# Kernel optimization log

Hardware: AMD Instinct MI355X
Metric: run time of the kernel (lower is better)

Reference implementation:

```python
import jax, jax.numpy as jnp
import numpy as np

JACCARD_THRESH = 0.5
NEG_POS = 3
VAR0, VAR1 = 0.1, 0.2
MAX_POS = 256  # static cap on gathered positives for the metric-learning terms


def point_form(boxes):
    # (cx,cy,w,h) -> (xmin,ymin,xmax,ymax)
    return jnp.concatenate([boxes[:, :2] - boxes[:, 2:] / 2,
                            boxes[:, :2] + boxes[:, 2:] / 2], axis=1)


def jaccard(a, b):
    # a: [O,4], b: [D,4] point form
    lt = jnp.maximum(a[:, None, :2], b[None, :, :2])
    rb = jnp.minimum(a[:, None, 2:], b[None, :, 2:])
    wh = jnp.clip(rb - lt, 0.0)
    inter = wh[..., 0] * wh[..., 1]
    area_a = (a[:, 2] - a[:, 0]) * (a[:, 3] - a[:, 1])
    area_b = (b[:, 2] - b[:, 0]) * (b[:, 3] - b[:, 1])
    return inter / (area_a[:, None] + area_b[None, :] - inter)


def encode(matched, priors):
    g_cxcy = ((matched[:, :2] + matched[:, 2:]) / 2 - priors[:, :2]) / (VAR0 * priors[:, 2:])
    g_wh = jnp.log((matched[:, 2:] - matched[:, :2]) / priors[:, 2:]) / VAR1
    return jnp.concatenate([g_cxcy, g_wh], axis=1)


def match_one(truths, labels, poses, priors):
    # standard SSD match (per image)
    ov = jaccard(truths, point_form(priors))          # [O, D]
    best_prior_idx = jnp.argmax(ov, axis=1)           # [O]
    best_truth_ov = jnp.max(ov, axis=0)               # [D]
    best_truth_idx = jnp.argmax(ov, axis=0)           # [D]
    best_truth_ov = best_truth_ov.at[best_prior_idx].set(2.0)
    best_truth_idx = best_truth_idx.at[best_prior_idx].set(jnp.arange(truths.shape[0]))
    matches = truths[best_truth_idx]                  # [D,4]
    conf = labels[best_truth_idx] + 1                 # background=0
    conf = jnp.where(best_truth_ov < JACCARD_THRESH, 0, conf)
    return encode(matches, priors), conf.astype(jnp.int32), poses[best_truth_idx]


def multibox_loss(loc_data, conf_data, line_data, pose_data, dbox_list, targets):
    B, D, C = conf_data.shape
    truths = targets[:, :, 0:4]
    labels = targets[:, :, 4].astype(jnp.int32)
    poses = targets[:, :, 5:8]
    loc_t, conf_t, pose_t = jax.vmap(match_one, in_axes=(0, 0, 0, None))(
        truths, labels, poses, dbox_list)

    pos = conf_t > 0                                  # [B,D]
    posf = pos.astype(loc_data.dtype)

    # smooth-L1 loc loss over positives (sum reduction)
    d = loc_data - loc_t
    sl1 = jnp.where(jnp.abs(d) < 1.0, 0.5 * d * d, jnp.abs(d) - 0.5)
    loss_l = jnp.sum(sl1 * posf[..., None])

    # pose squared-error over positives
    loss_p = jnp.sum((pose_data - pose_t) ** 2 * posf[..., None])

    # per-anchor cross entropy + hard-negative mining (double-argsort rank trick)
    logp = jax.nn.log_softmax(conf_data, axis=-1)
    ce = -jnp.take_along_axis(logp, conf_t[..., None], axis=-1)[..., 0]  # [B,D]
    ce_mined = jnp.where(pos, 0.0, ce)
    loss_idx = jnp.argsort(-ce_mined, axis=1)
    idx_rank = jnp.argsort(loss_idx, axis=1)
    num_pos = jnp.sum(pos.astype(jnp.int32), axis=1, keepdims=True)
    num_neg = jnp.minimum(num_pos * NEG_POS, D)
    neg = idx_rank < num_neg
    loss_c = jnp.sum(ce * (pos | neg).astype(ce.dtype))

    N = jnp.maximum(jnp.sum(posf), 1.0)
    loss_l = loss_l / N
    loss_c = loss_c / N
    loss_p = loss_p / N

    # ---- metric-learning block on gathered positives (static cap) ----
    pos_flat = pos.reshape(-1)
    order = jnp.argsort(jnp.where(pos_flat, 0, 1))[:MAX_POS]  # stable: row-major positives first
    valid = pos_flat[order]                                   # [K]
    emb = line_data.reshape(-1, line_data.shape[-1])[order]   # [K,32] raw embeddings
    lab = conf_t.reshape(-1)[order]                           # [K]
    qp = pose_t.reshape(-1, 3)[order]                         # [K,3]

    # PairMarginMiner / TripletMarginLoss use L2-normalized LpDistance by default
    nemb = emb / jnp.maximum(jnp.linalg.norm(emb, axis=1, keepdims=True), 1e-12)
    sq = jnp.sum((nemb[:, None, :] - nemb[None, :, :]) ** 2, axis=-1)
    dist = jnp.sqrt(jnp.maximum(sq, 1e-12))                   # [K,K]

    K = emb.shape[0]
    eye = jnp.eye(K, dtype=bool)
    vpair = valid[:, None] & valid[None, :] & ~eye
    same = lab[:, None] == lab[None, :]
    pos_pair = vpair & same & (dist > 0.2)   # mined hard positive pairs
    neg_pair = vpair & ~same & (dist < 0.8)  # mined hard negative pairs
    n_pp = jnp.sum(pos_pair)
    n_np = jnp.sum(neg_pair)

    # pairs -> triplets sharing the anchor; TripletMarginLoss(margin=0.2), AvgNonZero reducer
    trip_mask = pos_pair[:, :, None] & neg_pair[:, None, :]           # [K,K,K]
    trip_loss = jax.nn.relu(dist[:, :, None] - dist[:, None, :] + 0.2)
    nz = trip_mask & (trip_loss > 0)
    loss_t = jnp.sum(jnp.where(nz, trip_loss, 0.0)) / jnp.maximum(jnp.sum(nz), 1)

    # Ldesk over mined positive pairs: raw-embedding sq-dist vs pose sq-dist consistency
    e_sq = jnp.sum((emb[:, None, :] - emb[None, :, :]) ** 2, axis=-1)
    q_sq = jnp.sum((qp[:, None, :] - qp[None, :, :]) ** 2, axis=-1)
    desk_sum = jnp.sum(jnp.where(pos_pair, (e_sq - q_sq) ** 2, 0.0))
    npp = jnp.maximum(n_pp, 1).astype(loc_data.dtype)
    Ldesk = desk_sum / npp + loss_t / jnp.maximum(n_pp + n_np, 1)
    Ldesk = Ldesk / npp / 32.0

    return loss_l, loss_c, loss_p, Ldesk, loss_t


def setup_inputs():
    key = jax.random.key(0)
    ks = jax.random.split(key, 10)
    B, D, C, L, O = 32, 8732, 21, 32, 8
    loc_data = jax.random.normal(ks[0], (B, D, 4)) * 0.1
    conf_data = jax.random.normal(ks[1], (B, D, C))
    line_data = jax.random.normal(ks[2], (B, D, L))
    pose_data = jax.random.normal(ks[3], (B, D, 3))
    # default boxes (cx,cy,w,h) in (0,1)
    cxcy = jax.random.uniform(ks[4], (D, 2), minval=0.05, maxval=0.95)
    wh = jax.random.uniform(ks[5], (D, 2), minval=0.05, maxval=0.4)
    dbox_list = jnp.concatenate([cxcy, wh], axis=1)
    # targets: [xmin,ymin,xmax,ymax,label,pose(3),unused]
    mins = jax.random.uniform(ks[6], (B, O, 2), minval=0.0, maxval=0.6)
    sizes = jax.random.uniform(ks[7], (B, O, 2), minval=0.1, maxval=0.4)
    boxes = jnp.concatenate([mins, mins + sizes], axis=-1)
    labs = jax.random.randint(ks[8], (B, O, 1), 0, C - 1).astype(jnp.float32)
    pz = jax.random.normal(ks[9], (B, O, 3))
    targets = jnp.concatenate([boxes, labs, pz, jnp.zeros((B, O, 1))], axis=-1)
    return dict(loc_data=loc_data, conf_data=conf_data, line_data=line_data,
                pose_data=pose_data, dbox_list=dbox_list, targets=targets)


def reference(loc_data, conf_data, line_data, pose_data, dbox_list, targets):
    return multibox_loss(loc_data, conf_data, line_data, pose_data, dbox_list, targets)
```

## Files before the change

### kernel.cpp

```cpp
#include <hip/hip_runtime.h>
#include <cstdint>

#define B 32
#define D 8732
#define C 21
#define L 32
#define O 8
#define NSEGB 16
#define SEGLEN 546
#define NSEG 512
#define MT 576
#define NT 1024
#define PAIRB 128
#define TOPB 32
#define FINTGT (PAIRB + TOPB)

struct Ws {
  const float *loc, *conf, *line, *pose, *dbox, *targets;
  float* out;
  unsigned long long* bpPart;
  double* acc;
  int* ictr;
  int* cnt;
  int* posSlice;
  float* sce;
};

__device__ inline double waveSumD(double v) {
  #pragma unroll
  for (int s = 32; s > 0; s >>= 1) v += __shfl_down(v, s, 64);
  return v;
}

__device__ inline float iou_one(float tx1, float ty1, float tx2, float ty2, float ta,
                                float px1, float py1, float px2, float py2, float areaB) {
  float lx = fmaxf(tx1, px1), ly = fmaxf(ty1, py1);
  float rx = fminf(tx2, px2), ry = fminf(ry = ty2, py2);
  float iw = fmaxf(rx - lx, 0.f), ih = fmaxf(ry - ly, 0.f);
  float inter = iw * ih;
  return inter / (ta + areaB - inter);
}

__global__ __launch_bounds__(256) void k_bp(Ws p) {
  __shared__ float tb[O][4], ta[O];
  __shared__ unsigned long long wm[4][O];
  int g = blockIdx.x, tid = threadIdx.x;
  int lane = tid & 63, wav = tid >> 6;
  int b = g >> 4, s = g & 15;
  int dBeg = s * SEGLEN;
  int dEnd = dBeg + SEGLEN; if (dEnd > D) dEnd = D;
  if (g == 0) {
    if (tid < 9) p.acc[tid] = 0.0;
    if (tid == 9) { p.ictr[0] = 0; p.ictr[1] = 0; }
  }
  if (tid < O) {
    const float* tr = p.targets + ((size_t)b * O + tid) * 9;
    tb[tid][0] = tr[0]; tb[tid][1] = tr[1]; tb[tid][2] = tr[2]; tb[tid][3] = tr[3];
    ta[tid] = (tr[2] - tr[0]) * (tr[3] - tr[1]);
  }
  __syncthreads();
  float bi_[O]; int bd_[O];
  #pragma unroll
  for (int t = 0; t < O; t++) { bi_[t] = 0.f; bd_[t] = 0; }
  for (int d = dBeg + tid; d < dEnd; d += 256) {
    float4 db = *(const float4*)(p.dbox + (size_t)d * 4);
    float px1 = db.x - 0.5f*db.z, py1 = db.y - 0.5f*db.w;
    float px2 = db.x + 0.5f*db.z, py2 = db.y + 0.5f*db.w;
    float areaB = db.z * db.w;
    #pragma unroll
    for (int t = 0; t < O; t++) {
      float lx = fmaxf(tb[t][0], px1), ly = fmaxf(tb[t][1], py1);
      float rx = fminf(tb[t][2], px2), ry = fminf(tb[t][3], py2);
      float iw = fmaxf(rx - lx, 0.f), ih = fmaxf(ry - ly, 0.f);
      float inter = iw * ih;
      float iou = inter / (ta[t] + areaB - inter);
      if (iou > bi_[t]) { bi_[t] = iou; bd_[t] = d; }
    }
  }
  #pragma unroll
  for (int t = 0; t < O; t++) {
    unsigned long long k = ((unsigned long long)__float_as_uint(bi_[t]) << 32)
                         | (unsigned long long)(0xFFFFFFFFu - (unsigned)bd_[t]);
    #pragma unroll
    for (int sft = 32; sft > 0; sft >>= 1) {
      unsigned long long o = __shfl_down(k, sft, 64);
      if (o > k) k = o;
    }
    if (lane == 0) wm[wav][t] = k;
  }
  __syncthreads();
  if (tid < O) {
    unsigned long long k = wm[0][tid];
    #pragma unroll
    for (int w = 1; w < 4; w++) if (wm[w][tid] > k) k = wm[w][tid];
    p.bpPart[(size_t)g * O + tid] = k;
  }
}

struct ShM {
  float tb[O][4], ta[O], tl[O], tp_[O][3];
  unsigned long long bpred[128];
  int bpd[O];
  int plist[256];
  int wcnt[9], wbase[9];
  double wred[9][3];
  int run;
};

__global__ __launch_bounds__(MT, 4) void k_match(Ws p) {
  __shared__ ShM sh;
  int g = blockIdx.x, tid = threadIdx.x;
  int lane = tid & 63, wav = tid >> 6;
  int b = g >> 4, s = g & 15;
  int dBeg = s * SEGLEN;
  int dEnd = dBeg + SEGLEN; if (dEnd > D) dEnd = D;
  int d = dBeg + tid;
  bool act = d < dEnd;

  float x[C];
  if (act) {
    const float* cb = p.conf + ((size_t)b * D + d) * C;
    #pragma unroll
    for (int c = 0; c < C; c++) x[c] = cb[c];
  }
  if (tid < O) {
    const float* tr = p.targets + ((size_t)b * O + tid) * 9;
    sh.tb[tid][0] = tr[0]; sh.tb[tid][1] = tr[1];
    sh.tb[tid][2] = tr[2]; sh.tb[tid][3] = tr[3];
    sh.ta[tid] = (tr[2] - tr[0]) * (tr[3] - tr[1]);
    sh.tl[tid] = tr[4];
    sh.tp_[tid][0] = tr[5]; sh.tp_[tid][1] = tr[6]; sh.tp_[tid][2] = tr[7];
  }
  if (tid < 128)
    sh.bpred[tid] = p.bpPart[((size_t)b * NSEGB + (tid >> 3)) * O + (tid & 7)];
  __syncthreads();
  if (tid < O) {
    unsigned long long k = 0ull;
    #pragma unroll
    for (int s2 = 0; s2 < NSEGB; s2++) {
      unsigned long long kk = sh.bpred[s2 * 8 + tid];
      if (kk > k) k = kk;
    }
    sh.bpd[tid] = (int)(0xFFFFFFFFu - (unsigned)(k & 0xFFFFFFFFull));
  }
  __syncthreads();

  double ll = 0, lp = 0, cp = 0;
  int cls = 0, bi = 0;
  if (act) {
    float4 db = *(const float4*)(p.dbox + (size_t)d * 4);
    float px1 = db.x - 0.5f*db.z, py1 = db.y - 0.5f*db.w;
    float px2 = db.x + 0.5f*db.z, py2 = db.y + 0.5f*db.w;
    float areaB = db.z * db.w;
    float bv = -1.0f;
    #pragma unroll
    for (int t = 0; t < O; t++) {
      float iou = iou_one(sh.tb[t][0], sh.tb[t][1], sh.tb[t][2], sh.tb[t][3],
                          sh.ta[t], px1, py1, px2, py2, areaB);
      if (iou > bv) { bv = iou; bi = t; }
    }
    #pragma unroll
    for (int t = O - 1; t >= 0; t--)
      if (sh.bpd[t] == d) { bi = t; bv = 2.0f; break; }
    cls = (bv < 0.5f) ? 0 : ((int)sh.tl[bi] + 1);
    float m = x[0];
    #pragma unroll
    for (int c = 1; c < C; c++) m = fmaxf(m, x[c]);
    float sm = 0.f;
    #pragma unroll
    for (int c = 0; c < C; c++) sm += __expf(x[c] - m);
    float xc = x[0];
    #pragma unroll
    for (int c = 1; c < C; c++) xc = (cls == c) ? x[c] : xc;
    float ce = m + __logf(sm) - xc;
    size_t bd = (size_t)b * D + d;
    if (cls > 0) {
      cp += ce;
      p.sce[bd] = 0.f;
      float g0 = ((sh.tb[bi][0] + sh.tb[bi][2]) * 0.5f - db.x) / (0.1f * db.z);
      float g1 = ((sh.tb[bi][1] + sh.tb[bi][3]) * 0.5f - db.y) / (0.1f * db.w);
      float g2 = logf((sh.tb[bi][2] - sh.tb[bi][0]) / db.z) / 0.2f;
      float g3 = logf((sh.tb[bi][3] - sh.tb[bi][1]) / db.w) / 0.2f;
      float4 lo = *(const float4*)(p.loc + bd * 4);
      float dv, a;
      dv = lo.x - g0; a = fabsf(dv); ll += (double)((a < 1.f) ? 0.5f*dv*dv : a - 0.5f);
      dv = lo.y - g1; a = fabsf(dv); ll += (double)((a < 1.f) ? 0.5f*dv*dv : a - 0.5f);
      dv = lo.z - g2; a = fabsf(dv); ll += (double)((a < 1.f) ? 0.5f*dv*dv : a - 0.5f);
      dv = lo.w - g3; a = fabsf(dv); ll += (double)((a < 1.f) ? 0.5f*dv*dv : a - 0.5f);
      const float* po = p.pose + bd * 3;
      #pragma unroll
      for (int q = 0; q < 3; q++) {
        float pd = po[q] - sh.tp_[bi][q];
        lp += (double)pd * (double)pd;
      }
    } else {
      p.sce[bd] = fmaxf(ce, 0.f);
    }
  }

  const unsigned long long lt = (lane == 0) ? 0ull : (~0ull >> (64 - lane));
  bool pos = act && (cls > 0);
  unsigned long long mm = __ballot(pos);
  if (lane == 0) sh.wcnt[wav] = __popcll(mm);
  __syncthreads();
  if (tid == 0) {
    int r = 0;
    #pragma unroll
    for (int w = 0; w < 9; w++) { sh.wbase[w] = r; r += sh.wcnt[w]; }
    sh.run = r;
  }
  __syncthreads();
  if (pos) {
    int rank = sh.wbase[wav] + __popcll(mm & lt);
    if (rank < 256) sh.plist[rank] = d | (cls << 14) | (bi << 19);
  }
  __syncthreads();
  int tot = sh.run;
  if (tid == 0) p.cnt[g] = tot;
  int stored = (tot < 256) ? tot : 256;
  if (tid < stored) p.posSlice[g * 256 + tid] = sh.plist[tid];
  double a0 = waveSumD(ll), a1 = waveSumD(lp), a2 = waveSumD(cp);
  if (lane == 0) { sh.wred[wav][0] = a0; sh.wred[wav][1] = a1; sh.wred[wav][2] = a2; }
  __syncthreads();
  if (tid == 0) {
    double tll = 0, tlp = 0, tcp = 0;
    #pragma unroll
    for (int w = 0; w < 9; w++) { tll += sh.wred[w][0]; tlp += sh.wred[w][1]; tcp += sh.wred[w][2]; }
    atomicAdd(&p.acc[0], tll);
    atomicAdd(&p.acc[1], tlp);
    atomicAdd(&p.acc[2], tcp);
    atomicAdd(&p.ictr[0], tot);
  }
}

struct __align__(16) ShT {
  float sce[D];
  int whist[16][256];
  int hist[256];
  int scb[NSEGB];
  int nposS;
  unsigned prefixSh; int kkSh;
  double wsum[16], wcnt2[16];
};
struct ShP {
  float embT[L][256];
  float nembT[L][256];
  float qp_s[256][3];
  int   lab_s[256];
  float sd[2][256];
  int   Pi[NSEG + 1];
  int   wscan[8];
  unsigned long long spm[2][4], snm[2][4];
  double w1[2][4];
  int ppc[2][4], npc[2][4];
  double wS[16], wC[16];
};
struct ShD { int last; };
union Sh2 { ShT t; ShP pr; ShD dd; };

__global__ __launch_bounds__(NT) void k_minefin(Ws p) {
  __shared__ Sh2 sh;
  int g = blockIdx.x, tid = threadIdx.x;
  int lane = tid & 63, wav = tid >> 6;

  if (g >= PAIRB) {
    int bb = g - PAIRB;
    if (tid < NSEGB) sh.t.scb[tid] = p.cnt[bb * NSEGB + tid];
    const float* ce = p.sce + (size_t)bb * D;
    for (int i = tid; i < D / 4; i += NT)
      ((float4*)sh.t.sce)[i] = ((const float4*)ce)[i];
    __syncthreads();
    if (tid == 0) {
      int np = 0;
      #pragma unroll
      for (int q = 0; q < NSEGB; q++) np += sh.t.scb[q];
      sh.t.nposS = np;
    }
    __syncthreads();
    int npos = sh.t.nposS;
    int k = npos * 3; if (k > D) k = D;
    unsigned prefix = 0; int kk = k;
    for (int pass = 0; pass < 4; pass++) {
      int shift = 24 - 8 * pass;
      for (int i = tid; i < 16 * 256; i += NT) ((int*)sh.t.whist)[i] = 0;
      __syncthreads();
      unsigned himask = (pass == 0) ? 0u : (0xFFFFFFFFu << (shift + 8));
      for (int d = tid; d < D; d += NT) {
        unsigned keyb = __float_as_uint(sh.t.sce[d]);
        if ((keyb & himask) == (prefix & himask))
          atomicAdd(&sh.t.whist[wav][(keyb >> shift) & 255], 1);
      }
      __syncthreads();
      if (tid < 256) {
        int h = 0;
        #pragma unroll
        for (int w = 0; w < 16; w++) h += sh.t.whist[w][tid];
        sh.t.hist[tid] = h;
      }
      __syncthreads();
      if (tid < 64) {
        int l = tid;
        int h0 = sh.t.hist[l*4], h1 = sh.t.hist[l*4+1], h2 = sh.t.hist[l*4+2], h3 = sh.t.hist[l*4+3];
        int loc4 = h0 + h1 + h2 + h3;
        int suf = loc4;
        #pragma unroll
        for (int st = 1; st < 64; st <<= 1) {
          int o = __shfl_down(suf, st, 64);
          if (l + st < 64) suf += o;
        }
        int snext = suf - loc4;
        int s3 = snext + h3, s2 = s3 + h2, s1 = s2 + h1, s0 = s1 + h0;
        if (s3 >= kk && snext < kk) { sh.t.prefixSh = prefix | ((unsigned)(l*4+3) << shift); sh.t.kkSh = kk - snext; }
        if (s2 >= kk && s3 < kk)    { sh.t.prefixSh = prefix | ((unsigned)(l*4+2) << shift); sh.t.kkSh = kk - s3; }
        if (s1 >= kk && s2 < kk)    { sh.t.prefixSh = prefix | ((unsigned)(l*4+1) << shift); sh.t.kkSh = kk - s2; }
        if (s0 >= kk && s1 < kk)    { sh.t.prefixSh = prefix | ((unsigned)(l*4+0) << shift); sh.t.kkSh = kk - s1; }
      }
      __syncthreads();
      prefix = sh.t.prefixSh; kk = sh.t.kkSh;
      __syncthreads();
    }
    float T = __uint_as_float(prefix);
    double sgt = 0.0; int cgt = 0;
    for (int d = tid; d < D; d += NT) {
      float v = sh.t.sce[d];
      if (__float_as_uint(v) > prefix) { sgt += (double)v; cgt++; }
    }
    double wv = waveSumD(sgt);
    double wc = waveSumD((double)cgt);
    if (lane == 0) { sh.t.wsum[wav] = wv; sh.t.wcnt2[wav] = wc; }
    __syncthreads();
    if (tid == 0) {
      double tsg = 0, tcg = 0;
      #pragma unroll
      for (int w = 0; w < 16; w++) { tsg += sh.t.wsum[w]; tcg += sh.t.wcnt2[w]; }
      atomicAdd(&p.acc[3], tsg + ((double)k - tcg) * (double)T);
    }
  } else {
    int rgrp = tid >> 9;
    int i = 2 * g + rgrp;
    int t5 = tid & 511, j = t5 & 255, qq = t5 >> 8;

    int v = (tid < NSEG) ? p.cnt[tid] : 0;
    #pragma unroll
    for (int st = 1; st < 64; st <<= 1) {
      int o = __shfl_up(v, st, 64);
      if (lane >= st) v += o;
    }
    if (tid < NSEG && lane == 63) sh.pr.wscan[tid >> 6] = v;
    __syncthreads();
    if (tid < NSEG) {
      int add = 0;
      for (int q = 0; q < (tid >> 6); q++) add += sh.pr.wscan[q];
      sh.pr.Pi[tid + 1] = v + add;
    }
    if (tid == 0) sh.pr.Pi[0] = 0;
    __syncthreads();
    int total = sh.pr.Pi[NSEG];
    int Pc = (total < 256) ? total : 256;

    if (tid < 256) {
      int slot = tid;
      bool val = slot < Pc;
      int cls = 0, dpr = 0, seg = 0;
      float q0 = 0.f, q1 = 0.f, q2 = 0.f;
      if (val) {
        int lo = 0;
        #pragma unroll
        for (int st = 256; st > 0; st >>= 1) {
          int m = lo + st;
          if (m <= NSEG - 1 && sh.pr.Pi[m] <= slot) lo = m;
        }
        seg = lo;
        int idx = slot - sh.pr.Pi[seg];
        if (idx < 256) {
          int packed = p.posSlice[seg * 256 + idx];
          dpr = packed & 0x3FFF;
          cls = (packed >> 14) & 31;
          int bi = (packed >> 19) & 7;
          int bb2 = seg >> 4;
          const float* tr = p.targets + ((size_t)bb2 * O + bi) * 9;
          q0 = tr[5]; q1 = tr[6]; q2 = tr[7];
        } else val = false;
      }
      float nrm2 = 0.f;
      if (val) {
        int bb2 = seg >> 4;
        const float4* e4 = (const float4*)(p.line + ((size_t)bb2 * D + dpr) * L);
        #pragma unroll
        for (int c = 0; c < 8; c++) {
          float4 t4 = e4[c];
          sh.pr.embT[c*4+0][slot] = t4.x; sh.pr.embT[c*4+1][slot] = t4.y;
          sh.pr.embT[c*4+2][slot] = t4.z; sh.pr.embT[c*4+3][slot] = t4.w;
          nrm2 += t4.x*t4.x + t4.y*t4.y + t4.z*t4.z + t4.w*t4.w;
        }
      } else {
        #pragma unroll
        for (int c = 0; c < L; c++) sh.pr.embT[c][slot] = 0.f;
      }
      float inv = 1.f / fmaxf(sqrtf(nrm2), 1e-12f);
      #pragma unroll
      for (int c = 0; c < L; c++) sh.pr.nembT[c][slot] = sh.pr.embT[c][slot] * inv;
      sh.pr.lab_s[slot] = val ? cls : 0;
      sh.pr.qp_s[slot][0] = q0; sh.pr.qp_s[slot][1] = q1; sh.pr.qp_s[slot][2] = q2;
    }
    __syncthreads();

    int li = sh.pr.lab_s[i];
    bool vi = (i < Pc);
    bool pp = false, np = false;
    double dsk = 0.0;
    if (qq == 0) {
      bool vj = (j < Pc);
      float sq = 0.f, esq = 0.f;
      #pragma unroll
      for (int c = 0; c < L; c++) {
        float dn = sh.pr.nembT[c][i] - sh.pr.nembT[c][j];
        sq += dn * dn;
        float de = sh.pr.embT[c][i] - sh.pr.embT[c][j];
        esq += de * de;
      }
      float ddv = sqrtf(fmaxf(sq, 1e-12f));
      sh.pr.sd[rgrp][j] = ddv;
      float qsq = 0.f;
      #pragma unroll
      for (int c = 0; c < 3; c++) {
        float dq = sh.pr.qp_s[i][c] - sh.pr.qp_s[j][c];
        qsq += dq * dq;
      }
      bool vp = vi && vj && (i != j);
      bool same = (li == sh.pr.lab_s[j]);
      pp = vp && same && (ddv > 0.2f);
      np = vp && !same && (ddv < 0.8f);
      float diff = esq - qsq;
      dsk = pp ? (double)diff * (double)diff : 0.0;
    }
    unsigned long long pb = __ballot(pp), nb = __ballot(np);
    double dw = waveSumD(dsk);
    if (lane == 0 && qq == 0) {
      int w4 = wav & 3;
      sh.pr.spm[rgrp][w4] = pb; sh.pr.snm[rgrp][w4] = nb; sh.pr.w1[rgrp][w4] = dw;
      sh.pr.ppc[rgrp][w4] = (int)__popcll(pb); sh.pr.npc[rgrp][w4] = (int)__popcll(nb);
    }
    __syncthreads();
    unsigned long long pmw = sh.pr.spm[rgrp][j >> 6];
    bool pj = (pmw >> (j & 63)) & 1ull;
    float sdj = sh.pr.sd[rgrp][j];
    double ts = 0.0, tc = 0.0;
    if (pj) {
      for (int it = 0; it < 128; it++) {
        int kx = qq + 2 * it;
        unsigned long long nmw = sh.pr.snm[rgrp][kx >> 6];
        if ((nmw >> (kx & 63)) & 1ull) {
          float xv = sdj - sh.pr.sd[rgrp][kx] + 0.2f;
          if (xv > 0.f) { ts += (double)xv; tc += 1.0; }
        }
      }
    }
    ts = waveSumD(ts); tc = waveSumD(tc);
    if (lane == 0) { sh.pr.wS[wav] = ts; sh.pr.wC[wav] = tc; }
    __syncthreads();
    if (tid == 0) {
      double S = 0, Cc = 0;
      #pragma unroll
      for (int w = 0; w < 16; w++) { S += sh.pr.wS[w]; Cc += sh.pr.wC[w]; }
      double dsum = 0; int pcnt = 0, ncnt = 0;
      #pragma unroll
      for (int r = 0; r < 2; r++)
        #pragma unroll
        for (int w = 0; w < 4; w++) {
          dsum += sh.pr.w1[r][w]; pcnt += sh.pr.ppc[r][w]; ncnt += sh.pr.npc[r][w];
        }
      atomicAdd(&p.acc[4], dsum);
      atomicAdd(&p.acc[5], (double)pcnt);
      atomicAdd(&p.acc[6], (double)ncnt);
      atomicAdd(&p.acc[7], S);
      atomicAdd(&p.acc[8], Cc);
    }
  }

  if (tid == 0) {
    asm volatile("s_waitcnt vmcnt(0)" ::: "memory");
    int prev = __hip_atomic_fetch_add(&p.ictr[1], 1, __ATOMIC_RELAXED, __HIP_MEMORY_SCOPE_AGENT);
    sh.dd.last = (prev == FINTGT - 1);
  }
  __syncthreads();
  if (!sh.dd.last) return;
  if (tid == 0) {
    double lossL = __hip_atomic_load(&p.acc[0], __ATOMIC_RELAXED, __HIP_MEMORY_SCOPE_AGENT);
    double lossP = __hip_atomic_load(&p.acc[1], __ATOMIC_RELAXED, __HIP_MEMORY_SCOPE_AGENT);
    double ceP   = __hip_atomic_load(&p.acc[2], __ATOMIC_RELAXED, __HIP_MEMORY_SCOPE_AGENT);
    double ceN   = __hip_atomic_load(&p.acc[3], __ATOMIC_RELAXED, __HIP_MEMORY_SCOPE_AGENT);
    double desk  = __hip_atomic_load(&p.acc[4], __ATOMIC_RELAXED, __HIP_MEMORY_SCOPE_AGENT);
    double npp   = __hip_atomic_load(&p.acc[5], __ATOMIC_RELAXED, __HIP_MEMORY_SCOPE_AGENT);
    double nnp   = __hip_atomic_load(&p.acc[6], __ATOMIC_RELAXED, __HIP_MEMORY_SCOPE_AGENT);
    double tripS = __hip_atomic_load(&p.acc[7], __ATOMIC_RELAXED, __HIP_MEMORY_SCOPE_AGENT);
    double tripC = __hip_atomic_load(&p.acc[8], __ATOMIC_RELAXED, __HIP_MEMORY_SCOPE_AGENT);
    int nTotI    = __hip_atomic_load(&p.ictr[0], __ATOMIC_RELAXED, __HIP_MEMORY_SCOPE_AGENT);
    double N = (nTotI > 0) ? (double)nTotI : 1.0;
    p.out[0] = (float)(lossL / N);
    p.out[1] = (float)((ceP + ceN) / N);
    p.out[2] = (float)(lossP / N);
    double cnt = (tripC > 0.0) ? tripC : 1.0;
    double loss_t = tripS / cnt;
    double nppd = (npp > 0.0) ? npp : 1.0;
    double tot = npp + nnp;
    double denom = (tot > 0.0) ? tot : 1.0;
    double Ldesk = desk / nppd + loss_t / denom;
    Ldesk = Ldesk / nppd / 32.0;
    p.out[3] = (float)Ldesk;
    p.out[4] = (float)loss_t;
  }
}

extern "C" void kernel_launch(void* const* d_in, const int* in_sizes, int n_in,
                              void* d_out, int out_size, void* d_ws, size_t ws_size,
                              hipStream_t stream) {
  char* ws = (char*)d_ws;
  size_t off = 0;
  auto alloc = [&](size_t bytes) -> char* {
    char* q = ws + off;
    off += (bytes + 255) & ~(size_t)255;
    return q;
  };
  Ws p;
  p.loc     = (const float*)d_in[0];
  p.conf    = (const float*)d_in[1];
  p.line    = (const float*)d_in[2];
  p.pose    = (const float*)d_in[3];
  p.dbox    = (const float*)d_in[4];
  p.targets = (const float*)d_in[5];
  p.out     = (float*)d_out;
  p.bpPart   = (unsigned long long*)alloc((size_t)NSEG * O * 8);
  p.acc      = (double*)alloc(16 * 8);
  p.ictr     = (int*)alloc(256);
  p.cnt      = (int*)alloc(NSEG * 4);
  p.posSlice = (int*)alloc((size_t)NSEG * 256 * 4);
  p.sce      = (float*)alloc((size_t)B * D * 4);

  k_bp     <<<NSEG,  256, 0, stream>>>(p);
  k_match  <<<NSEG,  MT,  0, stream>>>(p);
  k_minefin<<<FINTGT, NT, 0, stream>>>(p);
}
```

Measured before the change: 149.3 us.

## Stage conf rows through LDS with coalesced loads; compute normalized embeddings on the fly

In k_match, each thread previously read its own 21-float conf row directly from global memory, a strided uncoalesced pattern. The block now copies the whole segment's conf slab into shared memory with coalesced float2 loads and threads read their rows from LDS. This adds about 46KB of shared memory and lowers the launch-bounds occupancy hint from 4 to 2. In the pair kernel, the normalized embedding copy is replaced by a per-slot inverse norm applied inside the distance loop, which halves shared-memory footprint and reads at the cost of a few extra multiplies.

```diff
diff --git a/kernel.cpp b/kernel.cpp
--- a/kernel.cpp
+++ b/kernel.cpp
@@ -35,7 +35,7 @@
 __device__ inline float iou_one(float tx1, float ty1, float tx2, float ty2, float ta,
                                 float px1, float py1, float px2, float py2, float areaB) {
   float lx = fmaxf(tx1, px1), ly = fmaxf(ty1, py1);
-  float rx = fminf(tx2, px2), ry = fminf(ry = ty2, py2);
+  float rx = fminf(tx2, px2), ry = fminf(ty2, py2);
   float iw = fmaxf(rx - lx, 0.f), ih = fmaxf(ry - ly, 0.f);
   float inter = iw * ih;
   return inter / (ta + areaB - inter);
@@ -69,11 +69,8 @@
     float areaB = db.z * db.w;
     #pragma unroll
     for (int t = 0; t < O; t++) {
-      float lx = fmaxf(tb[t][0], px1), ly = fmaxf(tb[t][1], py1);
-      float rx = fminf(tb[t][2], px2), ry = fminf(tb[t][3], py2);
-      float iw = fmaxf(rx - lx, 0.f), ih = fmaxf(ry - ly, 0.f);
-      float inter = iw * ih;
-      float iou = inter / (ta[t] + areaB - inter);
+      float iou = iou_one(tb[t][0], tb[t][1], tb[t][2], tb[t][3], ta[t],
+                          px1, py1, px2, py2, areaB);
       if (iou > bi_[t]) { bi_[t] = iou; bd_[t] = d; }
     }
   }
@@ -98,6 +95,7 @@
 }
 
 struct ShM {
+  float confS[SEGLEN * C];
   float tb[O][4], ta[O], tl[O], tp_[O][3];
   unsigned long long bpred[128];
   int bpd[O];
@@ -107,22 +105,17 @@
   int run;
 };
 
-__global__ __launch_bounds__(MT, 4) void k_match(Ws p) {
+__global__ __launch_bounds__(MT, 2) void k_match(Ws p) {
   __shared__ ShM sh;
   int g = blockIdx.x, tid = threadIdx.x;
   int lane = tid & 63, wav = tid >> 6;
   int b = g >> 4, s = g & 15;
   int dBeg = s * SEGLEN;
   int dEnd = dBeg + SEGLEN; if (dEnd > D) dEnd = D;
+  int segLen = dEnd - dBeg;
   int d = dBeg + tid;
-  bool act = d < dEnd;
-
-  float x[C];
-  if (act) {
-    const float* cb = p.conf + ((size_t)b * D + d) * C;
-    #pragma unroll
-    for (int c = 0; c < C; c++) x[c] = cb[c];
-  }
+  bool act = tid < segLen;
+
   if (tid < O) {
     const float* tr = p.targets + ((size_t)b * O + tid) * 9;
     sh.tb[tid][0] = tr[0]; sh.tb[tid][1] = tr[1];
@@ -133,6 +126,12 @@
   }
   if (tid < 128)
     sh.bpred[tid] = p.bpPart[((size_t)b * NSEGB + (tid >> 3)) * O + (tid & 7)];
+  {
+    const float2* csrc = (const float2*)(p.conf + ((size_t)b * D + dBeg) * C);
+    float2* cdst = (float2*)sh.confS;
+    int nf2 = (segLen * C) >> 1;
+    for (int i = tid; i < nf2; i += MT) cdst[i] = csrc[i];
+  }
   __syncthreads();
   if (tid < O) {
     unsigned long long k = 0ull;
@@ -148,6 +147,9 @@
   double ll = 0, lp = 0, cp = 0;
   int cls = 0, bi = 0;
   if (act) {
+    float x[C];
+    #pragma unroll
+    for (int c = 0; c < C; c++) x[c] = sh.confS[tid * C + c];
     float4 db = *(const float4*)(p.dbox + (size_t)d * 4);
     float px1 = db.x - 0.5f*db.z, py1 = db.y - 0.5f*db.w;
     float px2 = db.x + 0.5f*db.z, py2 = db.y + 0.5f*db.w;
@@ -244,7 +246,7 @@
 };
 struct ShP {
   float embT[L][256];
-  float nembT[L][256];
+  float invn[256];
   float qp_s[256][3];
   int   lab_s[256];
   float sd[2][256];
@@ -397,9 +399,7 @@
         #pragma unroll
         for (int c = 0; c < L; c++) sh.pr.embT[c][slot] = 0.f;
       }
-      float inv = 1.f / fmaxf(sqrtf(nrm2), 1e-12f);
-      #pragma unroll
-      for (int c = 0; c < L; c++) sh.pr.nembT[c][slot] = sh.pr.embT[c][slot] * inv;
+      sh.pr.invn[slot] = 1.f / fmaxf(sqrtf(nrm2), 1e-12f);
       sh.pr.lab_s[slot] = val ? cls : 0;
       sh.pr.qp_s[slot][0] = q0; sh.pr.qp_s[slot][1] = q1; sh.pr.qp_s[slot][2] = q2;
     }
@@ -411,13 +411,13 @@
     double dsk = 0.0;
     if (qq == 0) {
       bool vj = (j < Pc);
+      float invi = sh.pr.invn[i], invj = sh.pr.invn[j];
       float sq = 0.f, esq = 0.f;
       #pragma unroll
       for (int c = 0; c < L; c++) {
-        float dn = sh.pr.nembT[c][i] - sh.pr.nembT[c][j];
-        sq += dn * dn;
-        float de = sh.pr.embT[c][i] - sh.pr.embT[c][j];
-        esq += de * de;
+        float ei = sh.pr.embT[c][i], ej = sh.pr.embT[c][j];
+        float dn = ei * invi - ej * invj; sq += dn * dn;
+        float de = ei - ej;              esq += de * de;
       }
       float ddv = sqrtf(fmaxf(sq, 1e-12f));
       sh.pr.sd[rgrp][j] = ddv;
```

After: 149.2 us. Within noise of the previous version (-0.1%).
